# Kernel optimization log

Measured on AMD Instinct MI355X. Metric: run time of the kernel, lower is better.

Reference implementation:

```python
import jax, jax.numpy as jnp
import numpy as np

N_NODES = 12000
N_EDGES = 384000
F_IN = 128       # num_features
D = 64           # latent_dim (hidden_dim), num_gc_layers = 1
H_DEC = 64       # ceil(F_IN / 2)
BN_EPS = 1e-4


def _gcn_conv(x, W, b, src, dst, n):
    # PyG GCNConv: h = x @ W; add self-loops; sym-normalized scatter-add; + bias
    h = x @ W
    loop = jnp.arange(n)
    s = jnp.concatenate([src, loop])
    d = jnp.concatenate([dst, loop])
    deg = jax.ops.segment_sum(jnp.ones(s.shape[0], dtype=x.dtype), d, num_segments=n)
    dis = jax.lax.rsqrt(deg)  # deg >= 1 thanks to self-loops
    norm = dis[s] * dis[d]    # [E+N]
    out = jax.ops.segment_sum(h[s] * norm[:, None], d, num_segments=n)
    return out + b


def _bn_train(x, gamma, beta):
    # BatchNorm1d, training-mode batch statistics, biased variance, eps=1e-4
    mu = jnp.mean(x, axis=0)
    xc = x - mu
    var = jnp.mean(xc * xc, axis=0)
    return xc * jax.lax.rsqrt(var + BN_EPS) * gamma + beta


def _enc_layer(x, W, b, g, be, src, dst, n):
    # GCNConv -> Sigmoid -> (dropout no-op) -> BatchNorm
    return _bn_train(jax.nn.sigmoid(_gcn_conv(x, W, b, src, dst, n)), g, be)


def setup_inputs() -> dict:
    key = jax.random.key(0)
    ks = jax.random.split(key, 16)
    inp = {
        'x': jax.random.normal(ks[0], (N_NODES, F_IN), dtype=jnp.float32),
        'src': jax.random.randint(ks[1], (N_EDGES,), 0, N_NODES),
        'dst': jax.random.randint(ks[2], (N_EDGES,), 0, N_NODES),
        'batch': jnp.zeros((N_NODES,), dtype=jnp.int32),
        'noise': jax.random.normal(ks[3], (N_NODES, D), dtype=jnp.float32),
        # base_gcn encoder (GCNConv F_IN -> D, BN)
        'W0': jax.random.normal(ks[4], (F_IN, D), dtype=jnp.float32) * 0.08,
        'b0': jnp.zeros((D,), dtype=jnp.float32),
        'g0': jnp.ones((D,), dtype=jnp.float32),
        'be0': jnp.zeros((D,), dtype=jnp.float32),
        # gcn_mean encoder (GCNConv D -> D, BN)
        'Wm': jax.random.normal(ks[5], (D, D), dtype=jnp.float32) * 0.12,
        'bm': jnp.zeros((D,), dtype=jnp.float32),
        'gm': jnp.ones((D,), dtype=jnp.float32),
        'bem': jnp.zeros((D,), dtype=jnp.float32),
        # gcn_logstddev encoder (GCNConv D -> D, BN)
        'Ws': jax.random.normal(ks[6], (D, D), dtype=jnp.float32) * 0.12,
        'bs': jnp.zeros((D,), dtype=jnp.float32),
        'gs': jnp.ones((D,), dtype=jnp.float32),
        'bes': jnp.zeros((D,), dtype=jnp.float32),
        # decoder MLP: Linear(D, H_DEC) -> LeakyReLU -> Linear(H_DEC, F_IN)
        'Dw1': jax.random.normal(ks[7], (D, H_DEC), dtype=jnp.float32) * 0.12,
        'Db1': jnp.zeros((H_DEC,), dtype=jnp.float32),
        'Dw2': jax.random.normal(ks[8], (H_DEC, F_IN), dtype=jnp.float32) * 0.12,
        'Db2': jnp.zeros((F_IN,), dtype=jnp.float32),
    }
    return inp


def reference(x, src, dst, batch, noise,
              W0, b0, g0, be0,
              Wm, bm, gm, bem,
              Ws, bs, gs, bes,
              Dw1, Db1, Dw2, Db2):
    n = x.shape[0]
    hidden = _enc_layer(x, W0, b0, g0, be0, src, dst, n)          # [N, D]
    mean = _enc_layer(hidden, Wm, bm, gm, bem, src, dst, n)       # [N, D]
    logstd = _enc_layer(hidden, Ws, bs, gs, bes, src, dst, n)     # [N, D]
    z = noise * jnp.exp(logstd) + mean                            # reparam trick
    # decoder MLP (LeakyReLU default slope 0.01)
    h = jax.nn.leaky_relu(z @ Dw1 + Db1, negative_slope=0.01)
    reconstructed_x = h @ Dw2 + Db2                               # [N, F_IN]
    A_pred = jax.nn.sigmoid(z @ z.T)                              # [N, N]
    return (reconstructed_x, A_pred)
```

## Files before the change

kernel.cpp:

```cpp
#include <hip/hip_runtime.h>
#include <hip/hip_bf16.h>

#define N_NODES 12000
#define N_EDGES 384000
#define F_INN   128
#define DLAT    64
#define BN_EPS  1e-4f

typedef __attribute__((ext_vector_type(8))) short bf16x8;
typedef __attribute__((ext_vector_type(4))) float f32x4;

__device__ __forceinline__ float sigmoidf(float x) { return 1.0f / (1.0f + __expf(-x)); }

__device__ __forceinline__ unsigned short f2bf_rne(float x) {
    unsigned u = __float_as_uint(x);
    unsigned r = (u + 0x7fffu + ((u >> 16) & 1u)) >> 16;
    return (unsigned short)r;
}
__device__ __forceinline__ float bf2f(unsigned short h) {
    return __uint_as_float((unsigned)h << 16);
}

__global__ void k_init(int* cnt, int* cur, float* sA, float* sB,
                       unsigned short* zh, unsigned short* zl, int n) {
    int i = blockIdx.x * blockDim.x + threadIdx.x;
    if (i < n) { cnt[i] = 0; cur[i] = 0; }
    if (i < 128) sA[i] = 0.f;
    if (i < 256) sB[i] = 0.f;
    if (i < 2048) {
        zh[12000 * 64 + i] = 0;
        zl[12000 * 64 + i] = 0;
    }
}

__global__ void k_count(const int* dst, int* cnt, int e) {
    int i = blockIdx.x * blockDim.x + threadIdx.x;
    if (i < e) atomicAdd(&cnt[dst[i]], 1);
}

__global__ void k_scan(const int* __restrict__ cnt, int* __restrict__ offs,
                       float* __restrict__ dis, int n) {
    __shared__ int wsum[16];
    int tid = threadIdx.x;
    int base = tid * 12;
    int v[12];
    int s = 0;
#pragma unroll
    for (int q = 0; q < 12; q++) {
        int i = base + q;
        v[q] = (i < n) ? cnt[i] : 0;
        s += v[q];
        if (i < n) dis[i] = rsqrtf((float)(v[q] + 1));
    }
    int lane = tid & 63, w = tid >> 6;
    int ps = s;
#pragma unroll
    for (int o = 1; o < 64; o <<= 1) {
        int t2 = __shfl_up(ps, o, 64);
        if (lane >= o) ps += t2;
    }
    if (lane == 63) wsum[w] = ps;
    __syncthreads();
    if (tid == 0) {
        int acc = 0;
        for (int i = 0; i < 16; i++) { int t2 = wsum[i]; wsum[i] = acc; acc += t2; }
    }
    __syncthreads();
    int acc = wsum[w] + ps - s;
#pragma unroll
    for (int q = 0; q < 12; q++) {
        int i = base + q;
        if (i < n) offs[i] = acc;
        acc += v[q];
        if (i == n - 1) offs[n] = acc;
    }
}

__global__ void k_scatter(const int* src, const int* dst, const int* offs, int* cur,
                          int* ssrc, int e) {
    int i = blockIdx.x * blockDim.x + threadIdx.x;
    if (i < e) {
        int d = dst[i];
        int p = atomicAdd(&cur[d], 1);
        ssrc[offs[d] + p] = src[i];
    }
}

__global__ void k_mm(const float* __restrict__ X, int n, int K,
                     const float* __restrict__ Wa, int Ma,
                     const float* __restrict__ Wb, int Mb,
                     float* __restrict__ out) {
    __shared__ float Wl[8192];
    int M = Ma + Mb;
    for (int idx = threadIdx.x; idx < K * M; idx += blockDim.x) {
        int k = idx / M, m = idx % M;
        Wl[idx] = (m < Ma) ? Wa[k * Ma + m] : Wb[k * Mb + (m - Ma)];
    }
    __syncthreads();
    int rpb = blockDim.x / M;
    int r = blockIdx.x * rpb + threadIdx.x / M;
    int m = threadIdx.x % M;
    if (r >= n) return;
    const float* xr = X + (size_t)r * K;
    float acc = 0.f;
    for (int k = 0; k < K; k++) acc += xr[k] * Wl[k * M + m];
    out[(size_t)r * M + m] = acc;
}

__global__ void k_mm2bn(const float* __restrict__ X,
                        const float* __restrict__ sums,
                        const float* __restrict__ g0, const float* __restrict__ be0,
                        const float* __restrict__ Wa, const float* __restrict__ Wb,
                        float* __restrict__ out, int n) {
    __shared__ float Wl[64 * 128];
    __shared__ float bna[64], bnc[64];
    __shared__ float xs[2 * 64];
    int t = threadIdx.x;
    for (int idx = t; idx < 64 * 128; idx += 256) {
        int k = idx >> 7, m = idx & 127;
        Wl[idx] = (m < 64) ? Wa[k * 64 + m] : Wb[k * 64 + (m - 64)];
    }
    if (t < 64) {
        float mu = sums[t] / n;
        float var = sums[64 + t] / n - mu * mu;
        float a = rsqrtf(var + BN_EPS) * g0[t];
        bna[t] = a;
        bnc[t] = be0[t] - mu * a;
    }
    __syncthreads();
    if (t < 128) {
        int rr = t >> 6, k = t & 63;
        xs[rr * 64 + k] = X[(size_t)(blockIdx.x * 2 + rr) * 64 + k] * bna[k] + bnc[k];
    }
    __syncthreads();
    int r_loc = t >> 7, m = t & 127;
    int r = blockIdx.x * 2 + r_loc;
    float acc = 0.f;
    for (int k = 0; k < 64; k++) acc += xs[r_loc * 64 + k] * Wl[k * 128 + m];
    out[(size_t)r * 128 + m] = acc;
}

__global__ void k_agg(const float* __restrict__ h, const float* __restrict__ dis,
                      const int* __restrict__ offs, const int* __restrict__ ssrc,
                      const float* __restrict__ ba, const float* __restrict__ bb, int Ma,
                      float* __restrict__ out, int dim, int n) {
    int t = blockIdx.x * blockDim.x + threadIdx.x;
    int node = t / dim;
    if (node >= n) return;
    int f = t - node * dim;
    float di = dis[node];
    float acc = h[(size_t)node * dim + f] * di;
    int e0 = offs[node], e1 = offs[node + 1];
    int j = e0;
    for (; j + 3 < e1; j += 4) {
        int s0 = ssrc[j], s1 = ssrc[j + 1], s2 = ssrc[j + 2], s3 = ssrc[j + 3];
        acc += h[(size_t)s0 * dim + f] * dis[s0];
        acc += h[(size_t)s1 * dim + f] * dis[s1];
        acc += h[(size_t)s2 * dim + f] * dis[s2];
        acc += h[(size_t)s3 * dim + f] * dis[s3];
    }
    for (; j < e1; j++) {
        int s = ssrc[j];
        acc += h[(size_t)s * dim + f] * dis[s];
    }
    float bias = (f < Ma) ? ba[f] : bb[f - Ma];
    out[(size_t)node * dim + f] = sigmoidf(acc * di + bias);
}

#define STATS_BLOCKS 64
__global__ void k_stats1(const float* __restrict__ act, int dim, int n,
                         float* __restrict__ sums) {
    int rpb = 256 / dim;
    int c = threadIdx.x % dim;
    int rloc = threadIdx.x / dim;
    float s = 0.f, s2 = 0.f;
    for (int r = blockIdx.x * rpb + rloc; r < n; r += STATS_BLOCKS * rpb) {
        float v = act[(size_t)r * dim + c];
        s += v; s2 += v * v;
    }
    __shared__ float sh[512];
    sh[threadIdx.x] = s; sh[256 + threadIdx.x] = s2;
    __syncthreads();
    if (rloc == 0) {
        for (int q = 1; q < rpb; q++) {
            s += sh[q * dim + c];
            s2 += sh[256 + q * dim + c];
        }
        atomicAdd(&sums[c], s);
        atomicAdd(&sums[dim + c], s2);
    }
}

__global__ void k_zdec(const float* __restrict__ act2, const float* __restrict__ noise,
                       const float* __restrict__ sums,
                       const float* __restrict__ gm, const float* __restrict__ bem,
                       const float* __restrict__ gs, const float* __restrict__ bes,
                       const float* __restrict__ W1, const float* __restrict__ B1,
                       const float* __restrict__ W2, const float* __restrict__ B2,
                       unsigned short* __restrict__ zh, unsigned short* __restrict__ zl,
                       float* __restrict__ out, int n) {
    __shared__ float w1[64 * 64];
    __shared__ float w2[64 * 128];
    __shared__ float zs[16 * 64];
    __shared__ float hl[16 * 64];
    __shared__ float bnS[128], bnC[128];
    int t = threadIdx.x;
    int row0 = blockIdx.x * 16;
    {
        const float4* W14 = (const float4*)W1;
        const float4* W24 = (const float4*)W2;
        for (int i = t; i < 1024; i += 256) ((float4*)w1)[i] = W14[i];
        for (int i = t; i < 2048; i += 256) ((float4*)w2)[i] = W24[i];
    }
    if (t < 128) {
        float mu = sums[t] / n;
        float var = sums[128 + t] / n - mu * mu;
        float rs = rsqrtf(var + BN_EPS);
        float g  = (t < 64) ? gm[t] : gs[t - 64];
        float be = (t < 64) ? bem[t] : bes[t - 64];
        float a = rs * g;
        bnS[t] = a;
        bnC[t] = be - mu * a;
    }
    __syncthreads();
    {
        int base = t * 4;
        int row = base >> 6, j0 = base & 63;
        const float* ar = act2 + (size_t)(row0 + row) * 128;
        const float* nr = noise + (size_t)(row0 + row) * 64;
#pragma unroll
        for (int q = 0; q < 4; q++) {
            int j = j0 + q;
            float m  = ar[j]      * bnS[j]      + bnC[j];
            float ls = ar[64 + j] * bnS[64 + j] + bnC[64 + j];
            float zv = nr[j] * __expf(ls) + m;
            zs[row * 64 + j] = zv;
            unsigned short h = f2bf_rne(zv);
            size_t gi = (size_t)(row0 + row) * 64 + j;
            zh[gi] = h;
            zl[gi] = f2bf_rne(zv - bf2f(h));
        }
    }
    __syncthreads();
    {
        int hc = t & 63, rg = t >> 6;
        float a0 = B1[hc], a1 = a0, a2 = a0, a3 = a0;
        int rb = rg * 4;
        for (int k = 0; k < 64; k++) {
            float wv = w1[k * 64 + hc];
            a0 += zs[(rb + 0) * 64 + k] * wv;
            a1 += zs[(rb + 1) * 64 + k] * wv;
            a2 += zs[(rb + 2) * 64 + k] * wv;
            a3 += zs[(rb + 3) * 64 + k] * wv;
        }
        hl[(rb + 0) * 64 + hc] = a0 > 0.f ? a0 : 0.01f * a0;
        hl[(rb + 1) * 64 + hc] = a1 > 0.f ? a1 : 0.01f * a1;
        hl[(rb + 2) * 64 + hc] = a2 > 0.f ? a2 : 0.01f * a2;
        hl[(rb + 3) * 64 + hc] = a3 > 0.f ? a3 : 0.01f * a3;
    }
    __syncthreads();
    {
        int oc = t & 127, rg = t >> 7;
        float o[8];
#pragma unroll
        for (int i = 0; i < 8; i++) o[i] = B2[oc];
        int rb = rg * 8;
        for (int k = 0; k < 64; k++) {
            float wv = w2[k * 128 + oc];
#pragma unroll
            for (int i = 0; i < 8; i++) o[i] += hl[(rb + i) * 64 + k] * wv;
        }
#pragma unroll
        for (int i = 0; i < 8; i++)
            out[(size_t)(row0 + rb + i) * 128 + oc] = o[i];
    }
}

#define TN2 94
__global__ __launch_bounds__(256, 2) void k_apred(const unsigned short* __restrict__ zh,
                                                  const unsigned short* __restrict__ zl,
                                                  float* __restrict__ out, int n) {
    __shared__ __align__(16) unsigned short si_h[128 * 64];
    __shared__ __align__(16) unsigned short si_l[128 * 64];
    __shared__ __align__(16) unsigned short sj_h[128 * 64];
    __shared__ __align__(16) unsigned short sj_l[128 * 64];

    int bj = blockIdx.x, bi = blockIdx.y;
    int i0 = bi * 128, j0 = bj * 128;
    int t = threadIdx.x;

    auto stage = [&](const unsigned short* __restrict__ g, unsigned short* s, int row0) {
#pragma unroll
        for (int q = 0; q < 4; q++) {
            int u = q * 256 + t;
            int row = u >> 3, c16 = u & 7;
            int c16s = c16 ^ (row & 7);
            *(float4*)((char*)s + row * 128 + c16s * 16) =
                *(const float4*)(g + (size_t)(row0 + row) * 64 + c16 * 8);
        }
    };
    stage(zh, si_h, i0);
    stage(zl, si_l, i0);
    stage(zh, sj_h, j0);
    stage(zl, sj_l, j0);
    __syncthreads();

    int wave = t >> 6, lane = t & 63;
    int wr = wave >> 1, wc = wave & 1;
    int lrow = lane & 15;
    int kg   = lane >> 4;

    auto frag = [&](const unsigned short* s, int tr, int kc) -> bf16x8 {
        int c16s = (kc * 4 + kg) ^ (tr & 7);
        return *(const bf16x8*)((const char*)s + tr * 128 + c16s * 16);
    };

    f32x4 acc[4][4] = {};

#pragma unroll
    for (int kc = 0; kc < 2; kc++) {
        bf16x8 ah[4], al[4], bh[4], bl[4];
#pragma unroll
        for (int f = 0; f < 4; f++) {
            int tra = wr * 64 + f * 16 + lrow;
            ah[f] = frag(si_h, tra, kc);
            al[f] = frag(si_l, tra, kc);
            int trb = wc * 64 + f * 16 + lrow;
            bh[f] = frag(sj_h, trb, kc);
            bl[f] = frag(sj_l, trb, kc);
        }
#pragma unroll
        for (int fi = 0; fi < 4; fi++)
#pragma unroll
            for (int fj = 0; fj < 4; fj++) {
                acc[fi][fj] = __builtin_amdgcn_mfma_f32_16x16x32_bf16(
                    ah[fi], bh[fj], acc[fi][fj], 0, 0, 0);
                acc[fi][fj] = __builtin_amdgcn_mfma_f32_16x16x32_bf16(
                    ah[fi], bl[fj], acc[fi][fj], 0, 0, 0);
                acc[fi][fj] = __builtin_amdgcn_mfma_f32_16x16x32_bf16(
                    al[fi], bh[fj], acc[fi][fj], 0, 0, 0);
            }
    }

#pragma unroll
    for (int fi = 0; fi < 4; fi++)
#pragma unroll
        for (int fj = 0; fj < 4; fj++)
#pragma unroll
            for (int q = 0; q < 4; q++)
                acc[fi][fj][q] = sigmoidf(acc[fi][fj][q]);

    int colb = j0 + wc * 64;
#pragma unroll
    for (int fi = 0; fi < 4; fi++) {
#pragma unroll
        for (int q = 0; q < 4; q++) {
            int r = i0 + wr * 64 + fi * 16 + kg * 4 + q;
            if (r < n) {
                float* orow = out + (size_t)r * n + colb;
#pragma unroll
                for (int fj = 0; fj < 4; fj++) {
                    int c = fj * 16 + lrow;
                    if (colb + c < n)
                        __builtin_nontemporal_store(acc[fi][fj][q], &orow[c]);
                }
            }
        }
    }
}

extern "C" void kernel_launch(void* const* d_in, const int* in_sizes, int n_in,
                              void* d_out, int out_size, void* d_ws, size_t ws_size,
                              hipStream_t stream) {
    const float* x     = (const float*)d_in[0];
    const int*   src   = (const int*)d_in[1];
    const int*   dst   = (const int*)d_in[2];
    const float* noise = (const float*)d_in[4];
    const float* W0  = (const float*)d_in[5];
    const float* b0  = (const float*)d_in[6];
    const float* g0  = (const float*)d_in[7];
    const float* be0 = (const float*)d_in[8];
    const float* Wm  = (const float*)d_in[9];
    const float* bm  = (const float*)d_in[10];
    const float* gm  = (const float*)d_in[11];
    const float* bem = (const float*)d_in[12];
    const float* Ws  = (const float*)d_in[13];
    const float* bs  = (const float*)d_in[14];
    const float* gs  = (const float*)d_in[15];
    const float* bes = (const float*)d_in[16];
    const float* Dw1 = (const float*)d_in[17];
    const float* Db1 = (const float*)d_in[18];
    const float* Dw2 = (const float*)d_in[19];
    const float* Db2 = (const float*)d_in[20];
    float* out = (float*)d_out;

    const int n = N_NODES, e = N_EDGES;

    int*   cnt  = (int*)d_ws;
    int*   offs = (int*)d_ws + 12032;
    int*   cur  = (int*)d_ws + 24064;
    int*   ssrc = (int*)d_ws + 36096;
    float* dis  = (float*)d_ws + 420096;
    float* sA   = (float*)d_ws + 432128;
    float* sB   = (float*)d_ws + 432384;
    float* bufA = (float*)d_ws + 449024;
    float* bufB = bufA + (size_t)N_NODES * 128;
    unsigned short* zhbuf = (unsigned short*)((float*)d_ws + 3521024);
    unsigned short* zlbuf = (unsigned short*)((float*)d_ws + 3906048);

    k_init<<<(n + 255) / 256, 256, 0, stream>>>(cnt, cur, sA, sB, zhbuf, zlbuf, n);
    k_count<<<(e + 255) / 256, 256, 0, stream>>>(dst, cnt, e);
    k_scan<<<1, 1024, 0, stream>>>(cnt, offs, dis, n);
    k_scatter<<<(e + 255) / 256, 256, 0, stream>>>(src, dst, offs, cur, ssrc, e);

    k_mm<<<n / 4, 256, 0, stream>>>(x, n, F_INN, W0, DLAT, nullptr, 0, bufA);
    k_agg<<<(n * DLAT) / 256, 256, 0, stream>>>(bufA, dis, offs, ssrc, b0, nullptr, DLAT,
                                                bufB, DLAT, n);
    k_stats1<<<STATS_BLOCKS, 256, 0, stream>>>(bufB, DLAT, n, sA);

    k_mm2bn<<<n / 2, 256, 0, stream>>>(bufB, sA, g0, be0, Wm, Ws, bufA, n);
    k_agg<<<(n * 128) / 256, 256, 0, stream>>>(bufA, dis, offs, ssrc, bm, bs, DLAT,
                                               bufB, 128, n);
    k_stats1<<<STATS_BLOCKS, 256, 0, stream>>>(bufB, 128, n, sB);

    k_zdec<<<n / 16, 256, 0, stream>>>(bufB, noise, sB, gm, bem, gs, bes,
                                       Dw1, Db1, Dw2, Db2, zhbuf, zlbuf, out, n);

    {
        dim3 grid(TN2, TN2);
        k_apred<<<grid, 256, 0, stream>>>(zhbuf, zlbuf, out + (size_t)n * F_INN, n);
    }
}
```

Baseline: 902.2 us.

## Load A_pred fragments directly from global memory and remap blocks across XCDs

The A_pred kernel no longer stages the z tiles (high and low bf16 parts) into shared memory with a barrier. Each wave now loads its MFMA fragments straight from global memory, relying on L2 and L1 caching. The 2D grid becomes a 1D grid with an XCD-aware block remap, so neighbouring output tiles land on the same XCD and share L2. Launch bounds go from 2 to 3 blocks per CU. The kernel is dominated by writing the 12000x12000 fp32 output, so these changes mainly cut setup latency and LDS use, at the cost of redundant global fragment loads.

```diff
diff --git a/kernel.cpp b/kernel.cpp
--- a/kernel.cpp
+++ b/kernel.cpp
@@ -277,57 +277,40 @@
 }
 
 #define TN2 94
-__global__ __launch_bounds__(256, 2) void k_apred(const unsigned short* __restrict__ zh,
+__global__ __launch_bounds__(256, 3) void k_apred(const unsigned short* __restrict__ zh,
                                                   const unsigned short* __restrict__ zl,
                                                   float* __restrict__ out, int n) {
-    __shared__ __align__(16) unsigned short si_h[128 * 64];
-    __shared__ __align__(16) unsigned short si_l[128 * 64];
-    __shared__ __align__(16) unsigned short sj_h[128 * 64];
-    __shared__ __align__(16) unsigned short sj_l[128 * 64];
-
-    int bj = blockIdx.x, bi = blockIdx.y;
+    const int NB = TN2 * TN2;
+    int b = blockIdx.x;
+    int q = NB >> 3, r = NB & 7;
+    int xcd = b & 7, pos = b >> 3;
+    int wg = (xcd < r ? xcd * (q + 1) : r * (q + 1) + (xcd - r) * q) + pos;
+    int bi = wg / TN2, bj = wg % TN2;
     int i0 = bi * 128, j0 = bj * 128;
+
     int t = threadIdx.x;
-
-    auto stage = [&](const unsigned short* __restrict__ g, unsigned short* s, int row0) {
-#pragma unroll
-        for (int q = 0; q < 4; q++) {
-            int u = q * 256 + t;
-            int row = u >> 3, c16 = u & 7;
-            int c16s = c16 ^ (row & 7);
-            *(float4*)((char*)s + row * 128 + c16s * 16) =
-                *(const float4*)(g + (size_t)(row0 + row) * 64 + c16 * 8);
-        }
-    };
-    stage(zh, si_h, i0);
-    stage(zl, si_l, i0);
-    stage(zh, sj_h, j0);
-    stage(zl, sj_l, j0);
-    __syncthreads();
-
     int wave = t >> 6, lane = t & 63;
     int wr = wave >> 1, wc = wave & 1;
     int lrow = lane & 15;
     int kg   = lane >> 4;
 
-    auto frag = [&](const unsigned short* s, int tr, int kc) -> bf16x8 {
-        int c16s = (kc * 4 + kg) ^ (tr & 7);
-        return *(const bf16x8*)((const char*)s + tr * 128 + c16s * 16);
-    };
+    int arow0 = i0 + wr * 64;
+    int brow0 = j0 + wc * 64;
 
     f32x4 acc[4][4] = {};
 
 #pragma unroll
     for (int kc = 0; kc < 2; kc++) {
+        int koff = kc * 32 + kg * 8;
         bf16x8 ah[4], al[4], bh[4], bl[4];
 #pragma unroll
         for (int f = 0; f < 4; f++) {
-            int tra = wr * 64 + f * 16 + lrow;
-            ah[f] = frag(si_h, tra, kc);
-            al[f] = frag(si_l, tra, kc);
-            int trb = wc * 64 + f * 16 + lrow;
-            bh[f] = frag(sj_h, trb, kc);
-            bl[f] = frag(sj_l, trb, kc);
+            size_t aoff = (size_t)(arow0 + f * 16 + lrow) * 64 + koff;
+            ah[f] = *(const bf16x8*)(zh + aoff);
+            al[f] = *(const bf16x8*)(zl + aoff);
+            size_t boff = (size_t)(brow0 + f * 16 + lrow) * 64 + koff;
+            bh[f] = *(const bf16x8*)(zh + boff);
+            bl[f] = *(const bf16x8*)(zl + boff);
         }
 #pragma unroll
         for (int fi = 0; fi < 4; fi++)
@@ -347,22 +330,22 @@
 #pragma unroll
         for (int fj = 0; fj < 4; fj++)
 #pragma unroll
-            for (int q = 0; q < 4; q++)
-                acc[fi][fj][q] = sigmoidf(acc[fi][fj][q]);
+            for (int q2 = 0; q2 < 4; q2++)
+                acc[fi][fj][q2] = sigmoidf(acc[fi][fj][q2]);
 
     int colb = j0 + wc * 64;
 #pragma unroll
     for (int fi = 0; fi < 4; fi++) {
 #pragma unroll
-        for (int q = 0; q < 4; q++) {
-            int r = i0 + wr * 64 + fi * 16 + kg * 4 + q;
-            if (r < n) {
-                float* orow = out + (size_t)r * n + colb;
+        for (int q2 = 0; q2 < 4; q2++) {
+            int rr = i0 + wr * 64 + fi * 16 + kg * 4 + q2;
+            if (rr < n) {
+                float* orow = out + (size_t)rr * n + colb;
 #pragma unroll
                 for (int fj = 0; fj < 4; fj++) {
                     int c = fj * 16 + lrow;
                     if (colb + c < n)
-                        __builtin_nontemporal_store(acc[fi][fj][q], &orow[c]);
+                        __builtin_nontemporal_store(acc[fi][fj][q2], &orow[c]);
                 }
             }
         }
@@ -426,8 +409,5 @@
     k_zdec<<<n / 16, 256, 0, stream>>>(bufB, noise, sB, gm, bem, gs, bes,
                                        Dw1, Db1, Dw2, Db2, zhbuf, zlbuf, out, n);
 
-    {
-        dim3 grid(TN2, TN2);
-        k_apred<<<grid, 256, 0, stream>>>(zhbuf, zlbuf, out + (size_t)n * F_INN, n);
-    }
-}
+    k_apred<<<TN2 * TN2, 256, 0, stream>>>(zhbuf, zlbuf, out + (size_t)n * F_INN, n);
+}
```

Result: no change. 916.6 us (+1.6%).
